# Kernel tuning notes

Measured on AMD Instinct MI355X. Metric: run time of the kernel, lower is better.

The kernel has to match this reference:

```python
import jax, jax.numpy as jnp
import numpy as np

# Model dims (match init_kwargs)
D_MODEL = 768
EXPAND = 2
HEADDIM = 64
D_STATE = 64
D_CONV = 4
D_INNER = EXPAND * D_MODEL            # 1536 (== d_ssm, d_mlp = 0)
NHEADS = D_INNER // HEADDIM           # 24
CONV_DIM_PH = HEADDIM + 2 * D_STATE   # 192
CONV_DIM = NHEADS * CONV_DIM_PH       # 4608
D_IN_PROJ = D_INNER + CONV_DIM + NHEADS  # z + xBC + dt (d_mlp=0)

DT_MIN, DT_MAX = 1e-3, 1e-1


def setup_inputs() -> dict:
    key = jax.random.key(0)
    ks = jax.random.split(key, 12)
    B, L = 2, 2048
    s = 0.02
    # dt_bias init as in the torch module: inv_softplus of dt ~ loguniform(dt_min, dt_max)
    dt = jnp.exp(jax.random.uniform(ks[8], (NHEADS,)) * (np.log(DT_MAX) - np.log(DT_MIN)) + np.log(DT_MIN))
    dt = jnp.clip(dt, 1e-4, None)
    dt_bias = dt + jnp.log(-jnp.expm1(-dt))
    A_log = jnp.log(jax.random.uniform(ks[9], (NHEADS,), minval=1.0, maxval=16.0))
    return {
        "u": jax.random.normal(ks[0], (B, L, D_MODEL), jnp.float32),
        "W_in": jax.random.normal(ks[1], (D_IN_PROJ, D_MODEL), jnp.float32) * s,
        "conv_w": jax.random.normal(ks[2], (CONV_DIM, 1, D_CONV), jnp.float32) * 0.1,
        "conv_b": jnp.zeros((CONV_DIM,), jnp.float32),
        "R_x": jax.random.normal(ks[3], (NHEADS, HEADDIM, HEADDIM), jnp.float32) * 0.01,
        "R_B": jax.random.normal(ks[4], (NHEADS, D_STATE, HEADDIM), jnp.float32) * 0.01,
        "R_C": jax.random.normal(ks[5], (NHEADS, D_STATE, HEADDIM), jnp.float32) * 0.01,
        "R_dt": jax.random.normal(ks[6], (NHEADS, HEADDIM), jnp.float32) * 0.01,
        "dt_bias": dt_bias,
        "A_log": A_log,
        "D": jnp.ones((NHEADS, HEADDIM), jnp.float32),
        "W_out": jax.random.normal(ks[7], (D_MODEL, D_INNER), jnp.float32) * s,
    }


def reference(u, W_in, conv_w, conv_b, R_x, R_B, R_C, R_dt, dt_bias, A_log, D, W_out):
    B, L, _ = u.shape
    silu = jax.nn.silu

    # in_proj: split into SSM gate z, conv input xBC, dt pre-activation (d_mlp = 0)
    zxbcdt = u @ W_in.T                              # (B, L, D_IN_PROJ)
    z = zxbcdt[..., :D_INNER]                        # (B, L, d_ssm)
    xBC_in = zxbcdt[..., D_INNER:D_INNER + CONV_DIM] # (B, L, conv_dim)
    dt_raw = zxbcdt[..., D_INNER + CONV_DIM:]        # (B, L, NH)

    # causal depthwise conv1d (left-pad d_conv-1, truncate to L)
    xc = jax.lax.conv_general_dilated(
        xBC_in.transpose(0, 2, 1), conv_w,
        window_strides=(1,), padding=[(D_CONV - 1, 0)],
        dimension_numbers=("NCH", "OIH", "NCH"),
        feature_group_count=CONV_DIM) + conv_b[None, :, None]
    xBC_u = xc.transpose(0, 2, 1).reshape(B, L, NHEADS, CONV_DIM_PH)

    A = -jnp.exp(A_log)  # (NH,)

    def step(carry, inp):
        state, y_prev = carry            # (B,NH,DH,N), (B,NH,DH)
        xBC_t, dtr_t = inp               # (B,NH,DH+2N), (B,NH)
        x_u = xBC_t[..., :HEADDIM]
        B_u = xBC_t[..., HEADDIM:HEADDIM + D_STATE]
        C_u = xBC_t[..., HEADDIM + D_STATE:]
        # recurrent feedback of y_prev into x/B/C (pre-activation), then silu
        x = silu(x_u + jnp.einsum('hpq,bhq->bhp', R_x, y_prev))
        Bm = silu(B_u + jnp.einsum('hnq,bhq->bhn', R_B, y_prev))
        Cm = silu(C_u + jnp.einsum('hnq,bhq->bhn', R_C, y_prev))
        dt = jax.nn.softplus(dtr_t + jnp.einsum('hp,bhp->bh', R_dt, y_prev) + dt_bias)  # (B,NH)
        dA = jnp.exp(dt * A)             # (B,NH)
        state = state * dA[..., None, None] + (dt[..., None] * x)[..., None] * Bm[:, :, None, :]
        y = jnp.einsum('bhpn,bhn->bhp', state, Cm) + D * x   # (B,NH,DH)
        return (state, y), y

    state0 = jnp.zeros((B, NHEADS, HEADDIM, D_STATE), u.dtype)
    y0 = jnp.zeros((B, NHEADS, HEADDIM), u.dtype)
    xs = (xBC_u.transpose(1, 0, 2, 3), dt_raw.transpose(1, 0, 2))
    _, ys = jax.lax.scan(step, (state0, y0), xs)

    y = ys.transpose(1, 0, 2, 3)                              # (B,L,NH,DH)
    y = y * silu(z.reshape(B, L, NHEADS, HEADDIM))            # SSM gating
    out = y.reshape(B, L, D_INNER) @ W_out.T                  # (B,L,d_model)
    return out
```

## Files before the change

### kernel.cpp

```cpp
#include <hip/hip_runtime.h>

#define B_SZ    2
#define LSEQ    2048
#define DMODEL  768
#define DINNER  1536
#define NHEADS  24
#define HD      64
#define CDPH    192
#define CONVDIM 4608
#define DIP     6168
#define MROWS   (B_SZ*LSEQ)

typedef float f2 __attribute__((ext_vector_type(2)));
typedef float f32x4 __attribute__((ext_vector_type(4)));
typedef short bf16x8 __attribute__((ext_vector_type(8)));
typedef unsigned short us8 __attribute__((ext_vector_type(8)));

__device__ __forceinline__ float siluf(float x) {
    return x / (1.0f + __expf(-x));
}

#define WBAR() do { asm volatile("s_waitcnt lgkmcnt(0)" ::: "memory"); \
                    __builtin_amdgcn_s_barrier();                      \
                    asm volatile("" ::: "memory"); } while (0)

__device__ __forceinline__ float redux4(float v) {
    float a = v, b = v;
    asm("v_permlane16_swap_b32 %0, %1" : "+v"(a), "+v"(b));
    const float s = a + b;
    float c = s, d = s;
    asm("v_permlane32_swap_b32 %0, %1" : "+v"(c), "+v"(d));
    return c + d;
}

__device__ __forceinline__ ushort f2bf(float v) {
    uint u = __float_as_uint(v);
    return (ushort)((u + 0x7FFFu + ((u >> 16) & 1u)) >> 16);
}
__device__ __forceinline__ float bf2f(ushort h) {
    return __uint_as_float(((uint)h) << 16);
}

__global__ __launch_bounds__(256) void cvt_split(
    const float* __restrict__ in, ushort* __restrict__ hi,
    ushort* __restrict__ lo, int n4)
{
    int i = blockIdx.x * blockDim.x + threadIdx.x;
    const int stride = gridDim.x * blockDim.x;
    for (; i < n4; i += stride) {
        const float4 v = ((const float4*)in)[i];
        ushort4 h, l;
        h.x = f2bf(v.x); l.x = f2bf(v.x - bf2f(h.x));
        h.y = f2bf(v.y); l.y = f2bf(v.y - bf2f(h.y));
        h.z = f2bf(v.z); l.z = f2bf(v.z - bf2f(h.z));
        h.w = f2bf(v.w); l.w = f2bf(v.w - bf2f(h.w));
        ((ushort4*)hi)[i] = h;
        ((ushort4*)lo)[i] = l;
    }
}

template<int MODE>
__global__ __launch_bounds__(256) void gemm_nt_split(
    const float* __restrict__ A,
    const ushort* __restrict__ Ahi, const ushort* __restrict__ Alo,
    const float* __restrict__ B_,
    const ushort* __restrict__ Bhi, const ushort* __restrict__ Blo,
    float* __restrict__ C, int M, int N, int K)
{
    __shared__ ushort As_hi[128][56];
    __shared__ ushort As_lo[128][56];
    __shared__ ushort Bs_hi[128][56];
    __shared__ ushort Bs_lo[128][56];

    const int ntn = (N + 127) >> 7;
    const int bm = blockIdx.x / ntn;
    const int bn = blockIdx.x - bm * ntn;
    const int m0 = bm << 7, n0 = bn << 7;
    const int tid = threadIdx.x;
    const int wid = tid >> 6;
    const int l = tid & 63;
    const int wm = wid >> 1, wn = wid & 1;
    const int lr = l & 15;
    const int kq = l >> 4;

    const int srow = tid >> 1;
    const int scol = (tid & 1) << 4;
    const bool bok = (n0 + srow) < N;

    f32x4 acc[4][4];
#pragma unroll
    for (int i = 0; i < 4; ++i)
#pragma unroll
        for (int j = 0; j < 4; ++j) acc[i][j] = f32x4{0.f, 0.f, 0.f, 0.f};

    const size_t arow = (size_t)(m0 + srow) * K + scol;
    const size_t brow = (size_t)(n0 + srow) * K + scol;

    for (int k0 = 0; k0 < K; k0 += 32) {
        us8 ah0, ah1, al0, al1;
        float av[16];
        if constexpr (MODE >= 2) {
            ah0 = *(const us8*)(Ahi + arow + k0);
            ah1 = *(const us8*)(Ahi + arow + k0 + 8);
            al0 = *(const us8*)(Alo + arow + k0);
            al1 = *(const us8*)(Alo + arow + k0 + 8);
        } else {
#pragma unroll
            for (int q = 0; q < 4; ++q) {
                const float4 t = *(const float4*)(A + arow + k0 + q * 4);
                av[q*4+0] = t.x; av[q*4+1] = t.y;
                av[q*4+2] = t.z; av[q*4+3] = t.w;
            }
        }
        us8 bh0, bh1, bl0, bl1;
        float bv[16];
        if constexpr (MODE >= 1) {
            bh0 = us8{}; bh1 = us8{}; bl0 = us8{}; bl1 = us8{};
            if (bok) {
                bh0 = *(const us8*)(Bhi + brow + k0);
                bh1 = *(const us8*)(Bhi + brow + k0 + 8);
                bl0 = *(const us8*)(Blo + brow + k0);
                bl1 = *(const us8*)(Blo + brow + k0 + 8);
            }
        } else {
#pragma unroll
            for (int q = 0; q < 4; ++q) {
                float4 t = make_float4(0.f, 0.f, 0.f, 0.f);
                if (bok) t = *(const float4*)(B_ + brow + k0 + q * 4);
                bv[q*4+0] = t.x; bv[q*4+1] = t.y;
                bv[q*4+2] = t.z; bv[q*4+3] = t.w;
            }
        }
        __syncthreads();
        if constexpr (MODE >= 2) {
            *(us8*)&As_hi[srow][scol] = ah0; *(us8*)&As_hi[srow][scol + 8] = ah1;
            *(us8*)&As_lo[srow][scol] = al0; *(us8*)&As_lo[srow][scol + 8] = al1;
        } else {
#pragma unroll
            for (int q = 0; q < 16; ++q) {
                const ushort ah = f2bf(av[q]);
                As_hi[srow][scol + q] = ah;
                As_lo[srow][scol + q] = f2bf(av[q] - bf2f(ah));
            }
        }
        if constexpr (MODE >= 1) {
            *(us8*)&Bs_hi[srow][scol] = bh0; *(us8*)&Bs_hi[srow][scol + 8] = bh1;
            *(us8*)&Bs_lo[srow][scol] = bl0; *(us8*)&Bs_lo[srow][scol + 8] = bl1;
        } else {
#pragma unroll
            for (int q = 0; q < 16; ++q) {
                const ushort bh = f2bf(bv[q]);
                Bs_hi[srow][scol + q] = bh;
                Bs_lo[srow][scol + q] = f2bf(bv[q] - bf2f(bh));
            }
        }
        __syncthreads();

        bf16x8 ahf[4], alf[4], bhf[4], blf[4];
#pragma unroll
        for (int f = 0; f < 4; ++f) {
            const int ra = wm * 64 + f * 16 + lr;
            ahf[f] = *(const bf16x8*)&As_hi[ra][kq * 8];
            alf[f] = *(const bf16x8*)&As_lo[ra][kq * 8];
            const int rb = wn * 64 + f * 16 + lr;
            bhf[f] = *(const bf16x8*)&Bs_hi[rb][kq * 8];
            blf[f] = *(const bf16x8*)&Bs_lo[rb][kq * 8];
        }
#pragma unroll
        for (int i = 0; i < 4; ++i)
#pragma unroll
            for (int j = 0; j < 4; ++j) {
                acc[i][j] = __builtin_amdgcn_mfma_f32_16x16x32_bf16(
                    ahf[i], bhf[j], acc[i][j], 0, 0, 0);
                acc[i][j] = __builtin_amdgcn_mfma_f32_16x16x32_bf16(
                    ahf[i], blf[j], acc[i][j], 0, 0, 0);
                acc[i][j] = __builtin_amdgcn_mfma_f32_16x16x32_bf16(
                    alf[i], bhf[j], acc[i][j], 0, 0, 0);
            }
    }

#pragma unroll
    for (int i = 0; i < 4; ++i) {
#pragma unroll
        for (int j = 0; j < 4; ++j) {
            const int n = n0 + wn * 64 + j * 16 + lr;
            if (n < N) {
#pragma unroll
                for (int rg = 0; rg < 4; ++rg) {
                    const int m = m0 + wm * 64 + i * 16 + kq * 4 + rg;
                    C[(size_t)m * N + n] = acc[i][j][rg];
                }
            }
        }
    }
}

template<int WP>
__global__ __launch_bounds__(256, 1) void mamba_scanA(
    const float* __restrict__ zx,
    const float* __restrict__ conv_w,
    const float* __restrict__ conv_b,
    const float* __restrict__ R_x,
    const float* __restrict__ R_B,
    const float* __restrict__ R_C,
    const float* __restrict__ R_dt,
    const float* __restrict__ dt_bias,
    const float* __restrict__ A_log,
    const float* __restrict__ Dvec,
    float* __restrict__ yz,
    ushort* __restrict__ yzhi,
    ushort* __restrict__ yzlo)
{
    const int b = blockIdx.x / NHEADS;
    const int h = blockIdx.x % NHEADS;
    const int tid = threadIdx.x;
    const int w = tid >> 6;
    const int l = tid & 63;
    const int g = l >> 4;
    const int r = l & 15;
    const int p = (w << 4) + r;

    __shared__ __attribute__((aligned(16))) float ybuf[64];
    __shared__ __attribute__((aligned(16))) float Bml[64];
    __shared__ __attribute__((aligned(16))) float Cml[64];

    f2 Rx2[8], Rb2[8], Rc2[8], Rd2[8];
    {
        const size_t ro = ((size_t)h * 64 + p) * 64 + (g << 4);
#pragma unroll
        for (int q = 0; q < 4; ++q) {
            const float4 v = *(const float4*)(R_x + ro + q * 4);
            Rx2[q*2] = f2{v.x, v.y}; Rx2[q*2+1] = f2{v.z, v.w};
        }
#pragma unroll
        for (int q = 0; q < 4; ++q) {
            const float4 v = *(const float4*)(R_B + ro + q * 4);
            Rb2[q*2] = f2{v.x, v.y}; Rb2[q*2+1] = f2{v.z, v.w};
        }
#pragma unroll
        for (int q = 0; q < 4; ++q) {
            const float4 v = *(const float4*)(R_C + ro + q * 4);
            Rc2[q*2] = f2{v.x, v.y}; Rc2[q*2+1] = f2{v.z, v.w};
        }
#pragma unroll
        for (int q = 0; q < 4; ++q) {
            const float4 v = *(const float4*)(R_dt + h * 64 + (g << 4) + q * 4);
            Rd2[q*2] = f2{v.x, v.y}; Rd2[q*2+1] = f2{v.z, v.w};
        }
    }
    const float Aval = -__expf(A_log[h]);
    const float bias = dt_bias[h];
    const float Dp   = Dvec[h * 64 + p];

    float wx0, wx1, wx2, wx3, wb0, wb1, wb2, wb3, wc0, wc1, wc2, wc3;
    float cbx, cbB, cbC;
    {
        const float* cw = conv_w + (size_t)h * CDPH * 4;
        const float4 vx = *(const float4*)(cw + (size_t)p * 4);
        const float4 vb = *(const float4*)(cw + (size_t)(64 + p) * 4);
        const float4 vc = *(const float4*)(cw + (size_t)(128 + p) * 4);
        wx0 = vx.x; wx1 = vx.y; wx2 = vx.z; wx3 = vx.w;
        wb0 = vb.x; wb1 = vb.y; wb2 = vb.z; wb3 = vb.w;
        wc0 = vc.x; wc1 = vc.y; wc2 = vc.z; wc3 = vc.w;
        cbx = conv_b[h * CDPH + p];
        cbB = conv_b[h * CDPH + 64 + p];
        cbC = conv_b[h * CDPH + 128 + p];
    }
    float hx0 = 0.f, hx1 = 0.f, hx2 = 0.f;
    float hB0 = 0.f, hB1 = 0.f, hB2 = 0.f;
    float hC0 = 0.f, hC1 = 0.f, hC2 = 0.f;

    const float* xbc = zx + (size_t)b * LSEQ * DIP + DINNER + h * CDPH;
    const float* zb  = zx + (size_t)b * LSEQ * DIP + h * HD;
    const float* dtp = zx + (size_t)b * LSEQ * DIP + DINNER + CONVDIM + h;
    float*  yzb  = yz   + (size_t)b * LSEQ * DINNER + h * HD;
    ushort* yzhb = yzhi + (size_t)b * LSEQ * DINNER + h * HD;
    ushort* yzlb = yzlo + (size_t)b * LSEQ * DINNER + h * HD;

    f2 st2[8];
#pragma unroll
    for (int q = 0; q < 8; ++q) st2[q] = f2{0.f, 0.f};

    if (g == 0) ybuf[p] = 0.f;
    __syncthreads();

    float vx_c = xbc[p], vB_c = xbc[64 + p], vC_c = xbc[128 + p];
    float z_c = zb[p];
    float dtr_c = dtp[0];
    int off = DIP;

    for (int t = 0; t < LSEQ; ++t) {
        const float xcx = fmaf(wx3, vx_c, fmaf(wx2, hx2, fmaf(wx1, hx1, fmaf(wx0, hx0, cbx))));
        const float xcB = fmaf(wb3, vB_c, fmaf(wb2, hB2, fmaf(wb1, hB1, fmaf(wb0, hB0, cbB))));
        const float xcC = fmaf(wc3, vC_c, fmaf(wc2, hC2, fmaf(wc1, hC1, fmaf(wc0, hC0, cbC))));
        hx0 = hx1; hx1 = hx2; hx2 = vx_c;
        hB0 = hB1; hB1 = hB2; hB2 = vB_c;
        hC0 = hC1; hC1 = hC2; hC2 = vC_c;

        const float vx_n = xbc[off + p];
        const float vB_n = xbc[off + 64 + p];
        const float vC_n = xbc[off + 128 + p];
        const float z_n  = zb[off + p];
        const float dtr_n = dtp[off];
        const float zg = siluf(z_c);

        const float4* yb4 = (const float4*)(ybuf + (g << 4));
        f2 ax2 = {0.f, 0.f}, ab2 = {0.f, 0.f}, ac2 = {0.f, 0.f}, ad2 = {0.f, 0.f};
#pragma unroll
        for (int qq = 0; qq < 4; ++qq) {
            const float4 y4 = yb4[qq];
            const f2 ylo = {y4.x, y4.y}, yhi = {y4.z, y4.w};
            ax2 += Rx2[qq*2] * ylo; ax2 += Rx2[qq*2+1] * yhi;
            ab2 += Rb2[qq*2] * ylo; ab2 += Rb2[qq*2+1] * yhi;
            ac2 += Rc2[qq*2] * ylo; ac2 += Rc2[qq*2+1] * yhi;
            ad2 += Rd2[qq*2] * ylo; ad2 += Rd2[qq*2+1] * yhi;
        }
        const float ax = ax2.x + ax2.y, ab = ab2.x + ab2.y;
        const float ac = ac2.x + ac2.y, ad = ad2.x + ad2.y;

        const float Bm = siluf(xcB + redux4(ab));
        const float Cm = siluf(xcC + redux4(ac));
        if (g == 0) { Bml[p] = Bm; Cml[p] = Cm; }
        WBAR();

        const float4* bm4 = (const float4*)(Bml + (g << 4));
        const float4* cm4 = (const float4*)(Cml + (g << 4));
        const float4 bA = bm4[0], bB = bm4[1], bC = bm4[2], bD = bm4[3];
        const float4 cA = cm4[0], cB = cm4[1], cC = cm4[2], cD = cm4[3];

        const float xv = siluf(xcx + redux4(ax));
        const float dv = dtr_c + redux4(ad) + bias;
        const float dtv = (dv > 15.f) ? dv : __logf(1.f + __expf(dv));
        const float dAv = __expf(dtv * Aval);
        const float kx = dtv * xv;

        const f2 dA2 = {dAv, dAv};
        const f2 kx2 = {kx, kx};
        f2 bmv[8], cmv[8];
        bmv[0] = f2{bA.x, bA.y}; bmv[1] = f2{bA.z, bA.w};
        bmv[2] = f2{bB.x, bB.y}; bmv[3] = f2{bB.z, bB.w};
        bmv[4] = f2{bC.x, bC.y}; bmv[5] = f2{bC.z, bC.w};
        bmv[6] = f2{bD.x, bD.y}; bmv[7] = f2{bD.z, bD.w};
        cmv[0] = f2{cA.x, cA.y}; cmv[1] = f2{cA.z, cA.w};
        cmv[2] = f2{cB.x, cB.y}; cmv[3] = f2{cB.z, cB.w};
        cmv[4] = f2{cC.x, cC.y}; cmv[5] = f2{cC.z, cC.w};
        cmv[6] = f2{cD.x, cD.y}; cmv[7] = f2{cD.z, cD.w};
        f2 yp2 = {0.f, 0.f};
#pragma unroll
        for (int q = 0; q < 8; ++q) {
            st2[q] = st2[q] * dA2 + kx2 * bmv[q];
            yp2 += st2[q] * cmv[q];
        }
        const float ynew = redux4(yp2.x + yp2.y) + Dp * xv;

        if (g == 0) {
            ybuf[p] = ynew;
            if constexpr (WP) {
                const float o = ynew * zg;
                const ushort oh = f2bf(o);
                yzhb[p] = oh;
                yzlb[p] = f2bf(o - bf2f(oh));
            } else {
                yzb[p] = ynew * zg;
            }
        }
        WBAR();

        vx_c = vx_n; vB_c = vB_n; vC_c = vC_n; z_c = z_n; dtr_c = dtr_n;
        off += DIP;
        if constexpr (WP) { yzhb += DINNER; yzlb += DINNER; }
        else              { yzb += DINNER; }
    }
}

extern "C" void kernel_launch(void* const* d_in, const int* in_sizes, int n_in,
                              void* d_out, int out_size, void* d_ws, size_t ws_size,
                              hipStream_t stream) {
    const float* u       = (const float*)d_in[0];
    const float* W_in    = (const float*)d_in[1];
    const float* conv_w  = (const float*)d_in[2];
    const float* conv_b  = (const float*)d_in[3];
    const float* R_x     = (const float*)d_in[4];
    const float* R_B     = (const float*)d_in[5];
    const float* R_C     = (const float*)d_in[6];
    const float* R_dt    = (const float*)d_in[7];
    const float* dt_bias = (const float*)d_in[8];
    const float* A_log   = (const float*)d_in[9];
    const float* Dv      = (const float*)d_in[10];
    const float* W_out   = (const float*)d_in[11];
    float* out = (float*)d_out;

    const size_t ZXF = (size_t)MROWS * DIP;
    const size_t YZF = (size_t)MROWS * DINNER;
    const size_t UE  = (size_t)MROWS * DMODEL;
    const size_t WIE = (size_t)DIP * DMODEL;
    const size_t WOE = (size_t)DMODEL * DINNER;
    const size_t NEEDF = ZXF + UE + WIE + WOE + YZF;

    float* zx = (float*)d_ws;
    const bool pre = ws_size >= NEEDF * sizeof(float);

    if (pre) {
        float* pb = zx + ZXF;
        ushort* uhi  = (ushort*)pb;              ushort* ulo  = uhi + UE;
        ushort* wihi = (ushort*)(pb + UE);       ushort* wilo = wihi + WIE;
        ushort* wohi = (ushort*)(pb + UE + WIE); ushort* wolo = wohi + WOE;
        ushort* yzhi = (ushort*)(pb + UE + WIE + WOE);
        ushort* yzlo = yzhi + YZF;

        cvt_split<<<512, 256, 0, stream>>>(u, uhi, ulo, (int)(UE / 4));
        cvt_split<<<512, 256, 0, stream>>>(W_in, wihi, wilo, (int)(WIE / 4));
        cvt_split<<<512, 256, 0, stream>>>(W_out, wohi, wolo, (int)(WOE / 4));

        {
            const int M = MROWS, N = DIP, K = DMODEL;
            const int grid = (M / 128) * ((N + 127) / 128);
            gemm_nt_split<2><<<grid, 256, 0, stream>>>(
                nullptr, uhi, ulo, nullptr, wihi, wilo, zx, M, N, K);
        }
        mamba_scanA<1><<<B_SZ * NHEADS, 256, 0, stream>>>(
            zx, conv_w, conv_b, R_x, R_B, R_C, R_dt, dt_bias, A_log, Dv,
            nullptr, yzhi, yzlo);
        {
            const int M = MROWS, N = DMODEL, K = DINNER;
            const int grid = (M / 128) * ((N + 127) / 128);
            gemm_nt_split<2><<<grid, 256, 0, stream>>>(
                nullptr, yzhi, yzlo, nullptr, wohi, wolo, out, M, N, K);
        }
    } else {
        float* yz = zx + ZXF;
        {
            const int M = MROWS, N = DIP, K = DMODEL;
            const int grid = (M / 128) * ((N + 127) / 128);
            gemm_nt_split<0><<<grid, 256, 0, stream>>>(
                u, nullptr, nullptr, W_in, nullptr, nullptr, zx, M, N, K);
        }
        mamba_scanA<0><<<B_SZ * NHEADS, 256, 0, stream>>>(
            zx, conv_w, conv_b, R_x, R_B, R_C, R_dt, dt_bias, A_log, Dv,
            yz, nullptr, nullptr);
        {
            const int M = MROWS, N = DMODEL, K = DINNER;
            const int grid = (M / 128) * ((N + 127) / 128);
            gemm_nt_split<0><<<grid, 256, 0, stream>>>(
                yz, nullptr, nullptr, W_out, nullptr, nullptr, out, M, N, K);
        }
    }
}
```

Measured before the change: 1.970 ms.

## Remove mid-step barrier in scan by computing B/C redundantly per wave

Each wave now computes all 64 B and C feedback values itself, using four times as many R_B/R_C registers. Results are exchanged only through per-wave shared buffers, which drops one of the two block-wide barriers per timestep. The y and conv-input buffers are double-buffered, and the next step's conv is computed ahead of the barrier. The cost is four times the B/C matvec FMAs and much higher register pressure, which could cause spills.

Measured after the change: 2.963 ms. +50.4%, slower.

```diff
diff --git a/kernel.cpp b/kernel.cpp
--- a/kernel.cpp
+++ b/kernel.cpp
@@ -196,7 +196,7 @@
 }
 
 template<int WP>
-__global__ __launch_bounds__(256, 1) void mamba_scanA(
+__global__ __launch_bounds__(256, 1) void mamba_scanB(
     const float* __restrict__ zx,
     const float* __restrict__ conv_w,
     const float* __restrict__ conv_b,
@@ -220,32 +220,39 @@
     const int r = l & 15;
     const int p = (w << 4) + r;
 
-    __shared__ __attribute__((aligned(16))) float ybuf[64];
-    __shared__ __attribute__((aligned(16))) float Bml[64];
-    __shared__ __attribute__((aligned(16))) float Cml[64];
-
-    f2 Rx2[8], Rb2[8], Rc2[8], Rd2[8];
+    __shared__ __attribute__((aligned(16))) float ybuf[2][64];
+    __shared__ __attribute__((aligned(16))) float xcBl[2][64];
+    __shared__ __attribute__((aligned(16))) float xcCl[2][64];
+    __shared__ __attribute__((aligned(16))) float BW[4][64];
+    __shared__ __attribute__((aligned(16))) float CW[4][64];
+
+    f2 Rx2[8], Rd2[8], RB2[4][8], RC2[4][8];
     {
-        const size_t ro = ((size_t)h * 64 + p) * 64 + (g << 4);
+        const int ks = g << 4;
+        const size_t rox = ((size_t)h * 64 + p) * 64 + ks;
 #pragma unroll
         for (int q = 0; q < 4; ++q) {
-            const float4 v = *(const float4*)(R_x + ro + q * 4);
+            const float4 v = *(const float4*)(R_x + rox + q * 4);
             Rx2[q*2] = f2{v.x, v.y}; Rx2[q*2+1] = f2{v.z, v.w};
         }
 #pragma unroll
         for (int q = 0; q < 4; ++q) {
-            const float4 v = *(const float4*)(R_B + ro + q * 4);
-            Rb2[q*2] = f2{v.x, v.y}; Rb2[q*2+1] = f2{v.z, v.w};
-        }
-#pragma unroll
-        for (int q = 0; q < 4; ++q) {
-            const float4 v = *(const float4*)(R_C + ro + q * 4);
-            Rc2[q*2] = f2{v.x, v.y}; Rc2[q*2+1] = f2{v.z, v.w};
-        }
-#pragma unroll
-        for (int q = 0; q < 4; ++q) {
-            const float4 v = *(const float4*)(R_dt + h * 64 + (g << 4) + q * 4);
+            const float4 v = *(const float4*)(R_dt + h * 64 + ks + q * 4);
             Rd2[q*2] = f2{v.x, v.y}; Rd2[q*2+1] = f2{v.z, v.w};
+        }
+#pragma unroll
+        for (int j = 0; j < 4; ++j) {
+            const size_t ro = ((size_t)h * 64 + (j << 4) + r) * 64 + ks;
+#pragma unroll
+            for (int q = 0; q < 4; ++q) {
+                const float4 v = *(const float4*)(R_B + ro + q * 4);
+                RB2[j][q*2] = f2{v.x, v.y}; RB2[j][q*2+1] = f2{v.z, v.w};
+            }
+#pragma unroll
+            for (int q = 0; q < 4; ++q) {
+                const float4 v = *(const float4*)(R_C + ro + q * 4);
+                RC2[j][q*2] = f2{v.x, v.y}; RC2[j][q*2+1] = f2{v.z, v.w};
+            }
         }
     }
     const float Aval = -__expf(A_log[h]);
@@ -273,29 +280,34 @@
     const float* xbc = zx + (size_t)b * LSEQ * DIP + DINNER + h * CDPH;
     const float* zb  = zx + (size_t)b * LSEQ * DIP + h * HD;
     const float* dtp = zx + (size_t)b * LSEQ * DIP + DINNER + CONVDIM + h;
-    float*  yzb  = yz   + (size_t)b * LSEQ * DINNER + h * HD;
-    ushort* yzhb = yzhi + (size_t)b * LSEQ * DINNER + h * HD;
-    ushort* yzlb = yzlo + (size_t)b * LSEQ * DINNER + h * HD;
+    float*  yzb  = (WP == 0) ? yz   + (size_t)b * LSEQ * DINNER + h * HD : nullptr;
+    ushort* yzhb = (WP == 1) ? yzhi + (size_t)b * LSEQ * DINNER + h * HD : nullptr;
+    ushort* yzlb = (WP == 1) ? yzlo + (size_t)b * LSEQ * DINNER + h * HD : nullptr;
 
     f2 st2[8];
 #pragma unroll
     for (int q = 0; q < 8; ++q) st2[q] = f2{0.f, 0.f};
-
-    if (g == 0) ybuf[p] = 0.f;
-    __syncthreads();
 
     float vx_c = xbc[p], vB_c = xbc[64 + p], vC_c = xbc[128 + p];
     float z_c = zb[p];
     float dtr_c = dtp[0];
+
+    float xcx = fmaf(wx3, vx_c, cbx);
+    {
+        const float xcB0 = fmaf(wb3, vB_c, cbB);
+        const float xcC0 = fmaf(wc3, vC_c, cbC);
+        if (g == 0) {
+            xcBl[0][p] = xcB0; xcCl[0][p] = xcC0;
+            ybuf[0][p] = 0.f;
+        }
+    }
+    hx2 = vx_c; hB2 = vB_c; hC2 = vC_c;
+    __syncthreads();
+
     int off = DIP;
 
     for (int t = 0; t < LSEQ; ++t) {
-        const float xcx = fmaf(wx3, vx_c, fmaf(wx2, hx2, fmaf(wx1, hx1, fmaf(wx0, hx0, cbx))));
-        const float xcB = fmaf(wb3, vB_c, fmaf(wb2, hB2, fmaf(wb1, hB1, fmaf(wb0, hB0, cbB))));
-        const float xcC = fmaf(wc3, vC_c, fmaf(wc2, hC2, fmaf(wc1, hC1, fmaf(wc0, hC0, cbC))));
-        hx0 = hx1; hx1 = hx2; hx2 = vx_c;
-        hB0 = hB1; hB1 = hB2; hB2 = vB_c;
-        hC0 = hC1; hC1 = hC2; hC2 = vC_c;
+        const int cur = t & 1, nxt = cur ^ 1;
 
         const float vx_n = xbc[off + p];
         const float vB_n = xbc[off + 64 + p];
@@ -304,36 +316,54 @@
         const float dtr_n = dtp[off];
         const float zg = siluf(z_c);
 
-        const float4* yb4 = (const float4*)(ybuf + (g << 4));
-        f2 ax2 = {0.f, 0.f}, ab2 = {0.f, 0.f}, ac2 = {0.f, 0.f}, ad2 = {0.f, 0.f};
+        const float4* yb4 = (const float4*)(&ybuf[cur][g << 4]);
+        float cB0 = xcBl[cur][r],      cC0 = xcCl[cur][r];
+        float cB1 = xcBl[cur][16 + r], cC1 = xcCl[cur][16 + r];
+        float cB2 = xcBl[cur][32 + r], cC2 = xcCl[cur][32 + r];
+        float cB3 = xcBl[cur][48 + r], cC3 = xcCl[cur][48 + r];
+
+        f2 ax2 = {0.f,0.f}, ad2 = {0.f,0.f};
+        f2 ab_0 = {0.f,0.f}, ab_1 = {0.f,0.f}, ab_2 = {0.f,0.f}, ab_3 = {0.f,0.f};
+        f2 ac_0 = {0.f,0.f}, ac_1 = {0.f,0.f}, ac_2 = {0.f,0.f}, ac_3 = {0.f,0.f};
 #pragma unroll
         for (int qq = 0; qq < 4; ++qq) {
             const float4 y4 = yb4[qq];
             const f2 ylo = {y4.x, y4.y}, yhi = {y4.z, y4.w};
-            ax2 += Rx2[qq*2] * ylo; ax2 += Rx2[qq*2+1] * yhi;
-            ab2 += Rb2[qq*2] * ylo; ab2 += Rb2[qq*2+1] * yhi;
-            ac2 += Rc2[qq*2] * ylo; ac2 += Rc2[qq*2+1] * yhi;
-            ad2 += Rd2[qq*2] * ylo; ad2 += Rd2[qq*2+1] * yhi;
-        }
-        const float ax = ax2.x + ax2.y, ab = ab2.x + ab2.y;
-        const float ac = ac2.x + ac2.y, ad = ad2.x + ad2.y;
-
-        const float Bm = siluf(xcB + redux4(ab));
-        const float Cm = siluf(xcC + redux4(ac));
-        if (g == 0) { Bml[p] = Bm; Cml[p] = Cm; }
-        WBAR();
-
-        const float4* bm4 = (const float4*)(Bml + (g << 4));
-        const float4* cm4 = (const float4*)(Cml + (g << 4));
-        const float4 bA = bm4[0], bB = bm4[1], bC = bm4[2], bD = bm4[3];
-        const float4 cA = cm4[0], cB = cm4[1], cC = cm4[2], cD = cm4[3];
-
-        const float xv = siluf(xcx + redux4(ax));
-        const float dv = dtr_c + redux4(ad) + bias;
+            ax2  += Rx2[qq*2] * ylo;    ax2  += Rx2[qq*2+1] * yhi;
+            ad2  += Rd2[qq*2] * ylo;    ad2  += Rd2[qq*2+1] * yhi;
+            ab_0 += RB2[0][qq*2] * ylo; ab_0 += RB2[0][qq*2+1] * yhi;
+            ab_1 += RB2[1][qq*2] * ylo; ab_1 += RB2[1][qq*2+1] * yhi;
+            ab_2 += RB2[2][qq*2] * ylo; ab_2 += RB2[2][qq*2+1] * yhi;
+            ab_3 += RB2[3][qq*2] * ylo; ab_3 += RB2[3][qq*2+1] * yhi;
+            ac_0 += RC2[0][qq*2] * ylo; ac_0 += RC2[0][qq*2+1] * yhi;
+            ac_1 += RC2[1][qq*2] * ylo; ac_1 += RC2[1][qq*2+1] * yhi;
+            ac_2 += RC2[2][qq*2] * ylo; ac_2 += RC2[2][qq*2+1] * yhi;
+            ac_3 += RC2[3][qq*2] * ylo; ac_3 += RC2[3][qq*2+1] * yhi;
+        }
+
+        const float Bm0 = siluf(cB0 + redux4(ab_0.x + ab_0.y));
+        const float Bm1 = siluf(cB1 + redux4(ab_1.x + ab_1.y));
+        const float Bm2 = siluf(cB2 + redux4(ab_2.x + ab_2.y));
+        const float Bm3 = siluf(cB3 + redux4(ab_3.x + ab_3.y));
+        const float Cm0 = siluf(cC0 + redux4(ac_0.x + ac_0.y));
+        const float Cm1 = siluf(cC1 + redux4(ac_1.x + ac_1.y));
+        const float Cm2 = siluf(cC2 + redux4(ac_2.x + ac_2.y));
+        const float Cm3 = siluf(cC3 + redux4(ac_3.x + ac_3.y));
+        const float myB = (g & 1) ? ((g & 2) ? Bm3 : Bm1) : ((g & 2) ? Bm2 : Bm0);
+        const float myC = (g & 1) ? ((g & 2) ? Cm3 : Cm1) : ((g & 2) ? Cm2 : Cm0);
+        BW[w][l] = myB;
+        CW[w][l] = myC;
+
+        const float xv = siluf(xcx + redux4(ax2.x + ax2.y));
+        const float dv = dtr_c + redux4(ad2.x + ad2.y) + bias;
         const float dtv = (dv > 15.f) ? dv : __logf(1.f + __expf(dv));
         const float dAv = __expf(dtv * Aval);
         const float kx = dtv * xv;
 
+        const float4* bw4 = (const float4*)(&BW[w][g << 4]);
+        const float4* cw4 = (const float4*)(&CW[w][g << 4]);
+        const float4 bA = bw4[0], bB = bw4[1], bC = bw4[2], bD = bw4[3];
+        const float4 cA = cw4[0], cB = cw4[1], cC = cw4[2], cD = cw4[3];
         const f2 dA2 = {dAv, dAv};
         const f2 kx2 = {kx, kx};
         f2 bmv[8], cmv[8];
@@ -354,7 +384,7 @@
         const float ynew = redux4(yp2.x + yp2.y) + Dp * xv;
 
         if (g == 0) {
-            ybuf[p] = ynew;
+            ybuf[nxt][p] = ynew;
             if constexpr (WP) {
                 const float o = ynew * zg;
                 const ushort oh = f2bf(o);
@@ -364,6 +394,15 @@
                 yzb[p] = ynew * zg;
             }
         }
+
+        xcx = fmaf(wx3, vx_n, fmaf(wx2, hx2, fmaf(wx1, hx1, fmaf(wx0, hx0, cbx))));
+        const float xcBn = fmaf(wb3, vB_n, fmaf(wb2, hB2, fmaf(wb1, hB1, fmaf(wb0, hB0, cbB))));
+        const float xcCn = fmaf(wc3, vC_n, fmaf(wc2, hC2, fmaf(wc1, hC1, fmaf(wc0, hC0, cbC))));
+        hx0 = hx1; hx1 = hx2; hx2 = vx_n;
+        hB0 = hB1; hB1 = hB2; hB2 = vB_n;
+        hC0 = hC1; hC1 = hC2; hC2 = vC_n;
+        if (g == 0) { xcBl[nxt][p] = xcBn; xcCl[nxt][p] = xcCn; }
+
         WBAR();
 
         vx_c = vx_n; vB_c = vB_n; vC_c = vC_n; z_c = z_n; dtr_c = dtr_n;
@@ -418,7 +457,7 @@
             gemm_nt_split<2><<<grid, 256, 0, stream>>>(
                 nullptr, uhi, ulo, nullptr, wihi, wilo, zx, M, N, K);
         }
-        mamba_scanA<1><<<B_SZ * NHEADS, 256, 0, stream>>>(
+        mamba_scanB<1><<<B_SZ * NHEADS, 256, 0, stream>>>(
             zx, conv_w, conv_b, R_x, R_B, R_C, R_dt, dt_bias, A_log, Dv,
             nullptr, yzhi, yzlo);
         {
@@ -435,7 +474,7 @@
             gemm_nt_split<0><<<grid, 256, 0, stream>>>(
                 u, nullptr, nullptr, W_in, nullptr, nullptr, zx, M, N, K);
         }
-        mamba_scanA<0><<<B_SZ * NHEADS, 256, 0, stream>>>(
+        mamba_scanB<0><<<B_SZ * NHEADS, 256, 0, stream>>>(
             zx, conv_w, conv_b, R_x, R_B, R_C, R_dt, dt_bias, A_log, Dv,
             yz, nullptr, nullptr);
         {
```
